# Optimization experiments

Hardware: AMD Instinct MI355X
Metric: run time of the kernel (lower is better)

Reference implementation:

```python
import jax, jax.numpy as jnp
import numpy as np
from jax import lax

NUM_EXPERTS = 64
HIDDEN = 1024
INTERMEDIATE = 768
TOTAL_TOKENS = 8192


def setup_inputs() -> dict:
    key = jax.random.key(0)
    k1, k2, k3, k4 = jax.random.split(key, 4)
    x = jax.random.normal(k1, (TOTAL_TOKENS, HIDDEN), dtype=jnp.float32)
    scale = 0.02
    w1 = jax.random.normal(k2, (NUM_EXPERTS, HIDDEN, INTERMEDIATE), dtype=jnp.float32) * scale
    w2 = jax.random.normal(k3, (NUM_EXPERTS, INTERMEDIATE, HIDDEN), dtype=jnp.float32) * scale
    w3 = jax.random.normal(k4, (NUM_EXPERTS, HIDDEN, INTERMEDIATE), dtype=jnp.float32) * scale
    # Variable tokens per expert, summing exactly to TOTAL_TOKENS (tokens are pre-sorted by expert).
    counts = np.random.default_rng(0).multinomial(TOTAL_TOKENS, [1.0 / NUM_EXPERTS] * NUM_EXPERTS)
    num_tokens_per_expert = jnp.asarray(counts, dtype=jnp.int32)
    return {"x": x, "w1": w1, "w2": w2, "w3": w3,
            "num_tokens_per_expert": num_tokens_per_expert}


def reference(x, w1, w2, w3, num_tokens_per_expert):
    """SwiGLU grouped-expert FFN: down(silu(gate(x)) * up(x)), grouped by expert.

    x: (T, H) tokens sorted by expert; num_tokens_per_expert: (E,) int32.
    Matches torch._grouped_mm semantics: compute in bfloat16, cast back to x.dtype.
    """
    gs = num_tokens_per_expert.astype(jnp.int32)
    xb = x.astype(jnp.bfloat16)
    w1b = w1.astype(jnp.bfloat16)
    w2b = w2.astype(jnp.bfloat16)
    w3b = w3.astype(jnp.bfloat16)
    gate = lax.ragged_dot(xb, w1b, gs)          # (T, I) grouped GEMM
    up = lax.ragged_dot(xb, w3b, gs)            # (T, I)
    h = jax.nn.silu(gate) * up                  # fused SwiGLU activation
    out = lax.ragged_dot(h, w2b, gs)            # (T, H)
    return out.astype(x.dtype)
```

## Files before the change

kernel.cpp:

```cpp
#include <hip/hip_runtime.h>
#include <stdint.h>

#define E_ 64
#define H_ 1024
#define I_ 768
#define T_ 8192

typedef __attribute__((ext_vector_type(4))) float floatx4;
typedef __attribute__((ext_vector_type(8))) short bf16x8;

__device__ inline unsigned short f2bf(float f) {
  union { float f; uint32_t u; } v; v.f = f;
  return (unsigned short)((v.u + 0x7FFFu + ((v.u >> 16) & 1u)) >> 16);
}
__device__ inline float bf2f(unsigned short s) {
  union { uint32_t u; float f; } v; v.u = ((uint32_t)s) << 16;
  return v.f;
}

__device__ inline void gload16(const void* g, void* l) {
  __builtin_amdgcn_global_load_lds(
      (const __attribute__((address_space(1))) void*)g,
      (__attribute__((address_space(3))) void*)l, 16, 0, 0);
}

__global__ void k_prep(const float* __restrict__ x, unsigned short* __restrict__ xb,
                       const int* __restrict__ cnts, int* __restrict__ offs) {
  int i = blockIdx.x * 256 + threadIdx.x;
  float4 v = ((const float4*)x)[i];
  ushort4 o;
  o.x = f2bf(v.x); o.y = f2bf(v.y); o.z = f2bf(v.z); o.w = f2bf(v.w);
  ((ushort4*)xb)[i] = o;
  if (i == 0) {
    int s = 0; offs[0] = 0;
    for (int e = 0; e < E_; ++e) { s += cnts[e]; offs[e + 1] = s; }
  }
}

__global__ __launch_bounds__(256, 2) void k_gemm1(
    const unsigned short* __restrict__ xb, const float* __restrict__ w1,
    const float* __restrict__ w3, unsigned short* __restrict__ h,
    const int* __restrict__ offs) {
  __shared__ unsigned short As[2][256 * 32];
  __shared__ float Bs1[2][32 * 64];
  __shared__ float Bs3[2][32 * 64];

  const int tid = threadIdx.x;
  const int wv = tid >> 6;
  const int l = tid & 63;
  const int lq = l >> 4;
  const int ln = l & 15;
  const int e = blockIdx.x / (I_ / 64);
  const int n0 = (blockIdx.x % (I_ / 64)) * 64;
  const int off = offs[e];
  const int cnt = offs[e + 1] - off;

  const float* b1p = w1 + (size_t)e * (H_ * I_) + (size_t)(tid >> 4) * I_ + n0 + (tid & 15) * 4;
  const float* b3p = w3 + (size_t)e * (H_ * I_) + (size_t)(tid >> 4) * I_ + n0 + (tid & 15) * 4;

  for (int mb = 0; mb < cnt; mb += 256) {
    const int m_here = (cnt - mb) < 256 ? (cnt - mb) : 256;
    const bool active = (wv * 64) < m_here;

    const unsigned short* aptr[4];
#pragma unroll
    for (int r = 0; r < 4; ++r) {
      int row = off + mb + r * 64 + (tid >> 2);
      row = row < (T_ - 1) ? row : (T_ - 1);
      aptr[r] = xb + (size_t)row * H_ + (tid & 3) * 8;
    }

    auto STG = [&](int kt, int buf) {
#pragma unroll
      for (int r = 0; r < 4; ++r)
        gload16(aptr[r] + kt * 32, &As[buf][tid * 8 + r * 2048]);
#pragma unroll
      for (int r = 0; r < 2; ++r) {
        gload16(b1p + (size_t)(kt * 32 + r * 16) * I_, &Bs1[buf][tid * 4 + r * 1024]);
        gload16(b3p + (size_t)(kt * 32 + r * 16) * I_, &Bs3[buf][tid * 4 + r * 1024]);
      }
    };

    floatx4 accG[4][4], accU[4][4];
#pragma unroll
    for (int i2 = 0; i2 < 4; ++i2)
#pragma unroll
      for (int j2 = 0; j2 < 4; ++j2) {
        accG[i2][j2] = (floatx4){0.f, 0.f, 0.f, 0.f};
        accU[i2][j2] = (floatx4){0.f, 0.f, 0.f, 0.f};
      }

    const int NK = H_ / 32;
    STG(0, 0);
    for (int kt = 0; kt < NK; ++kt) {
      const int cur = kt & 1;
      if (kt + 1 < NK) {
        STG(kt + 1, cur ^ 1);
        asm volatile("s_waitcnt vmcnt(8)" ::: "memory");
      } else {
        asm volatile("s_waitcnt vmcnt(0)" ::: "memory");
      }
      __builtin_amdgcn_s_barrier();
      asm volatile("" ::: "memory");

      if (active) {
        const unsigned short* Asc = As[cur];
        const float* B1c = Bs1[cur];
        const float* B3c = Bs3[cur];
        bf16x8 bG[4], bU[4];
#pragma unroll
        for (int nf = 0; nf < 4; ++nf) {
          const float* p1 = &B1c[(lq * 8) * 64 + nf * 16 + ln];
          const float* p3 = &B3c[(lq * 8) * 64 + nf * 16 + ln];
          bf16x8 t1, t3;
#pragma unroll
          for (int j = 0; j < 8; ++j) {
            t1[j] = (short)f2bf(p1[j * 64]);
            t3[j] = (short)f2bf(p3[j * 64]);
          }
          bG[nf] = t1; bU[nf] = t3;
        }
#pragma unroll
        for (int mf = 0; mf < 4; ++mf) {
          const bf16x8 af = *(const bf16x8*)&Asc[(size_t)(wv * 64 + mf * 16 + ln) * 32 + lq * 8];
#pragma unroll
          for (int nf = 0; nf < 4; ++nf) {
            accG[mf][nf] = __builtin_amdgcn_mfma_f32_16x16x32_bf16(af, bG[nf], accG[mf][nf], 0, 0, 0);
            accU[mf][nf] = __builtin_amdgcn_mfma_f32_16x16x32_bf16(af, bU[nf], accU[mf][nf], 0, 0, 0);
          }
        }
      }
      asm volatile("" ::: "memory");
      __builtin_amdgcn_s_barrier();
    }

    if (active) {
#pragma unroll
      for (int mf = 0; mf < 4; ++mf)
#pragma unroll
        for (int nf = 0; nf < 4; ++nf)
#pragma unroll
          for (int r = 0; r < 4; ++r) {
            int row_l = wv * 64 + mf * 16 + lq * 4 + r;
            if (row_l < m_here) {
              float g = bf2f(f2bf(accG[mf][nf][r]));
              float u = bf2f(f2bf(accU[mf][nf][r]));
              float hv = (g / (1.0f + __expf(-g))) * u;
              h[(size_t)(off + mb + row_l) * I_ + n0 + nf * 16 + ln] = f2bf(hv);
            }
          }
    }
    asm volatile("s_waitcnt vmcnt(0)" ::: "memory");
  }
}

__global__ __launch_bounds__(256, 3) void k_gemm2(
    const unsigned short* __restrict__ h, const float* __restrict__ w2,
    float* __restrict__ out, const int* __restrict__ offs) {
  __shared__ unsigned short As[2][256 * 32];
  __shared__ float Bs[2][32 * 64];

  const int tid = threadIdx.x;
  const int wv = tid >> 6;
  const int l = tid & 63;
  const int lq = l >> 4;
  const int ln = l & 15;
  const int e = blockIdx.x / (H_ / 64);
  const int n0 = (blockIdx.x % (H_ / 64)) * 64;
  const int off = offs[e];
  const int cnt = offs[e + 1] - off;

  const float* b2p = w2 + (size_t)e * (I_ * H_) + (size_t)(tid >> 4) * H_ + n0 + (tid & 15) * 4;

  for (int mb = 0; mb < cnt; mb += 256) {
    const int m_here = (cnt - mb) < 256 ? (cnt - mb) : 256;
    const bool active = (wv * 64) < m_here;

    const unsigned short* aptr[4];
#pragma unroll
    for (int r = 0; r < 4; ++r) {
      int row = off + mb + r * 64 + (tid >> 2);
      row = row < (T_ - 1) ? row : (T_ - 1);
      aptr[r] = h + (size_t)row * I_ + (tid & 3) * 8;
    }

    auto STG = [&](int kt, int buf) {
#pragma unroll
      for (int r = 0; r < 4; ++r)
        gload16(aptr[r] + kt * 32, &As[buf][tid * 8 + r * 2048]);
#pragma unroll
      for (int r = 0; r < 2; ++r)
        gload16(b2p + (size_t)(kt * 32 + r * 16) * H_, &Bs[buf][tid * 4 + r * 1024]);
    };

    floatx4 acc[4][4];
#pragma unroll
    for (int i2 = 0; i2 < 4; ++i2)
#pragma unroll
      for (int j2 = 0; j2 < 4; ++j2) acc[i2][j2] = (floatx4){0.f, 0.f, 0.f, 0.f};

    const int NK = I_ / 32;
    STG(0, 0);
    for (int kt = 0; kt < NK; ++kt) {
      const int cur = kt & 1;
      if (kt + 1 < NK) {
        STG(kt + 1, cur ^ 1);
        asm volatile("s_waitcnt vmcnt(6)" ::: "memory");
      } else {
        asm volatile("s_waitcnt vmcnt(0)" ::: "memory");
      }
      __builtin_amdgcn_s_barrier();
      asm volatile("" ::: "memory");

      if (active) {
        const unsigned short* Asc = As[cur];
        const float* Bc = Bs[cur];
        bf16x8 bF[4];
#pragma unroll
        for (int nf = 0; nf < 4; ++nf) {
          const float* p = &Bc[(lq * 8) * 64 + nf * 16 + ln];
          bf16x8 t;
#pragma unroll
          for (int j = 0; j < 8; ++j) t[j] = (short)f2bf(p[j * 64]);
          bF[nf] = t;
        }
#pragma unroll
        for (int mf = 0; mf < 4; ++mf) {
          const bf16x8 af = *(const bf16x8*)&Asc[(size_t)(wv * 64 + mf * 16 + ln) * 32 + lq * 8];
#pragma unroll
          for (int nf = 0; nf < 4; ++nf)
            acc[mf][nf] = __builtin_amdgcn_mfma_f32_16x16x32_bf16(af, bF[nf], acc[mf][nf], 0, 0, 0);
        }
      }
      asm volatile("" ::: "memory");
      __builtin_amdgcn_s_barrier();
    }

    if (active) {
#pragma unroll
      for (int mf = 0; mf < 4; ++mf)
#pragma unroll
        for (int nf = 0; nf < 4; ++nf)
#pragma unroll
          for (int r = 0; r < 4; ++r) {
            int row_l = wv * 64 + mf * 16 + lq * 4 + r;
            if (row_l < m_here)
              out[(size_t)(off + mb + row_l) * H_ + n0 + nf * 16 + ln] = acc[mf][nf][r];
          }
    }
    asm volatile("s_waitcnt vmcnt(0)" ::: "memory");
  }
}

extern "C" void kernel_launch(void* const* d_in, const int* in_sizes, int n_in,
                              void* d_out, int out_size, void* d_ws, size_t ws_size,
                              hipStream_t stream) {
  const float* x  = (const float*)d_in[0];
  const float* w1 = (const float*)d_in[1];
  const float* w2 = (const float*)d_in[2];
  const float* w3 = (const float*)d_in[3];
  const int* cnts = (const int*)d_in[4];
  float* out = (float*)d_out;

  char* ws = (char*)d_ws;
  int* offs = (int*)ws;
  unsigned short* xb = (unsigned short*)(ws + 1024);
  unsigned short* h  = (unsigned short*)(ws + 1024 + (size_t)T_ * H_ * 2);

  k_prep<<<(T_ * H_) / (256 * 4), 256, 0, stream>>>(x, xb, cnts, offs);
  k_gemm1<<<E_ * (I_ / 64), 256, 0, stream>>>(xb, w1, w3, h, offs);
  k_gemm2<<<E_ * (H_ / 64), 256, 0, stream>>>(h, w2, out, offs);
}
```

Before: 628.7 us.

## Load A fragments directly to registers and convert B to bf16 once per tile

Both GEMM kernels stop staging the activation tile in LDS and load A fragments straight from global memory into registers. The fp32 weight tile is converted cooperatively into a swizzled bf16 LDS buffer once per k-step, instead of every wave converting it redundantly. The B prefetch becomes two tiles deep, and the block index is remapped across groups of eight. This cuts LDS footprint and redundant conversion work, but adds a second barrier per k-step and exposes global A-load latency inside the loop.

```diff
diff --git a/kernel.cpp b/kernel.cpp
--- a/kernel.cpp
+++ b/kernel.cpp
@@ -23,6 +23,8 @@
       (const __attribute__((address_space(1))) void*)g,
       (__attribute__((address_space(3))) void*)l, 16, 0, 0);
 }
+
+__device__ inline int bslot(int n, int c) { return n * 4 + (c ^ ((n >> 1) & 3)); }
 
 __global__ void k_prep(const float* __restrict__ x, unsigned short* __restrict__ xb,
                        const int* __restrict__ cnts, int* __restrict__ offs) {
@@ -41,19 +43,22 @@
     const unsigned short* __restrict__ xb, const float* __restrict__ w1,
     const float* __restrict__ w3, unsigned short* __restrict__ h,
     const int* __restrict__ offs) {
-  __shared__ unsigned short As[2][256 * 32];
-  __shared__ float Bs1[2][32 * 64];
-  __shared__ float Bs3[2][32 * 64];
+  __shared__ __align__(16) float Bf[2][2][32 * 64];
+  __shared__ __align__(16) unsigned short Bh[2][64 * 32];
 
   const int tid = threadIdx.x;
   const int wv = tid >> 6;
   const int l = tid & 63;
   const int lq = l >> 4;
   const int ln = l & 15;
-  const int e = blockIdx.x / (I_ / 64);
-  const int n0 = (blockIdx.x % (I_ / 64)) * 64;
+  const int bid = ((int)blockIdx.x & 7) * (E_ * (I_ / 64) / 8) + ((int)blockIdx.x >> 3);
+  const int e = bid / (I_ / 64);
+  const int n0 = (bid % (I_ / 64)) * 64;
   const int off = offs[e];
   const int cnt = offs[e + 1] - off;
+
+  const int cn = tid & 63;
+  const int ck = tid >> 6;
 
   const float* b1p = w1 + (size_t)e * (H_ * I_) + (size_t)(tid >> 4) * I_ + n0 + (tid & 15) * 4;
   const float* b3p = w3 + (size_t)e * (H_ * I_) + (size_t)(tid >> 4) * I_ + n0 + (tid & 15) * 4;
@@ -62,22 +67,19 @@
     const int m_here = (cnt - mb) < 256 ? (cnt - mb) : 256;
     const bool active = (wv * 64) < m_here;
 
-    const unsigned short* aptr[4];
-#pragma unroll
-    for (int r = 0; r < 4; ++r) {
-      int row = off + mb + r * 64 + (tid >> 2);
+    const unsigned short* aF[4];
+#pragma unroll
+    for (int mf = 0; mf < 4; ++mf) {
+      int row = off + mb + wv * 64 + mf * 16 + ln;
       row = row < (T_ - 1) ? row : (T_ - 1);
-      aptr[r] = xb + (size_t)row * H_ + (tid & 3) * 8;
-    }
-
-    auto STG = [&](int kt, int buf) {
-#pragma unroll
-      for (int r = 0; r < 4; ++r)
-        gload16(aptr[r] + kt * 32, &As[buf][tid * 8 + r * 2048]);
+      aF[mf] = xb + (size_t)row * H_ + lq * 8;
+    }
+
+    auto STGB = [&](int kt, int buf) {
 #pragma unroll
       for (int r = 0; r < 2; ++r) {
-        gload16(b1p + (size_t)(kt * 32 + r * 16) * I_, &Bs1[buf][tid * 4 + r * 1024]);
-        gload16(b3p + (size_t)(kt * 32 + r * 16) * I_, &Bs3[buf][tid * 4 + r * 1024]);
+        gload16(b1p + (size_t)(kt * 32 + r * 16) * I_, &Bf[buf][0][tid * 4 + r * 1024]);
+        gload16(b3p + (size_t)(kt * 32 + r * 16) * I_, &Bf[buf][1][tid * 4 + r * 1024]);
       }
     };
 
@@ -91,47 +93,55 @@
       }
 
     const int NK = H_ / 32;
-    STG(0, 0);
+    STGB(0, 0);
+    STGB(1, 1);
     for (int kt = 0; kt < NK; ++kt) {
       const int cur = kt & 1;
-      if (kt + 1 < NK) {
-        STG(kt + 1, cur ^ 1);
-        asm volatile("s_waitcnt vmcnt(8)" ::: "memory");
-      } else {
-        asm volatile("s_waitcnt vmcnt(0)" ::: "memory");
-      }
-      __builtin_amdgcn_s_barrier();
-      asm volatile("" ::: "memory");
-
-      if (active) {
-        const unsigned short* Asc = As[cur];
-        const float* B1c = Bs1[cur];
-        const float* B3c = Bs3[cur];
+      if (kt == NK - 1) asm volatile("s_waitcnt vmcnt(0)" ::: "memory");
+      else              asm volatile("s_waitcnt vmcnt(4)" ::: "memory");
+      __builtin_amdgcn_s_barrier();
+      asm volatile("" ::: "memory");
+
+#pragma unroll
+      for (int m = 0; m < 2; ++m) {
+        uint32_t dw[4];
+#pragma unroll
+        for (int d = 0; d < 4; ++d) {
+          float v0 = Bf[cur][m][(ck * 8 + 2 * d) * 64 + cn];
+          float v1 = Bf[cur][m][(ck * 8 + 2 * d + 1) * 64 + cn];
+          dw[d] = (uint32_t)f2bf(v0) | ((uint32_t)f2bf(v1) << 16);
+        }
+        *(uint4*)&Bh[m][(size_t)bslot(cn, ck) * 8] = make_uint4(dw[0], dw[1], dw[2], dw[3]);
+      }
+      asm volatile("s_waitcnt lgkmcnt(0)" ::: "memory");
+      __builtin_amdgcn_s_barrier();
+      asm volatile("" ::: "memory");
+
+      bf16x8 af[4];
+      if (active) {
+#pragma unroll
+        for (int mf = 0; mf < 4; ++mf) af[mf] = *(const bf16x8*)(aF[mf] + kt * 32);
+      }
+      asm volatile("" ::: "memory");
+      if (kt + 2 < NK) STGB(kt + 2, cur);
+      asm volatile("" ::: "memory");
+
+      if (active) {
         bf16x8 bG[4], bU[4];
 #pragma unroll
         for (int nf = 0; nf < 4; ++nf) {
-          const float* p1 = &B1c[(lq * 8) * 64 + nf * 16 + ln];
-          const float* p3 = &B3c[(lq * 8) * 64 + nf * 16 + ln];
-          bf16x8 t1, t3;
-#pragma unroll
-          for (int j = 0; j < 8; ++j) {
-            t1[j] = (short)f2bf(p1[j * 64]);
-            t3[j] = (short)f2bf(p3[j * 64]);
+          const int sl = bslot(nf * 16 + ln, lq) * 8;
+          bG[nf] = *(const bf16x8*)&Bh[0][sl];
+          bU[nf] = *(const bf16x8*)&Bh[1][sl];
+        }
+#pragma unroll
+        for (int mf = 0; mf < 4; ++mf)
+#pragma unroll
+          for (int nf = 0; nf < 4; ++nf) {
+            accG[mf][nf] = __builtin_amdgcn_mfma_f32_16x16x32_bf16(af[mf], bG[nf], accG[mf][nf], 0, 0, 0);
+            accU[mf][nf] = __builtin_amdgcn_mfma_f32_16x16x32_bf16(af[mf], bU[nf], accU[mf][nf], 0, 0, 0);
           }
-          bG[nf] = t1; bU[nf] = t3;
-        }
-#pragma unroll
-        for (int mf = 0; mf < 4; ++mf) {
-          const bf16x8 af = *(const bf16x8*)&Asc[(size_t)(wv * 64 + mf * 16 + ln) * 32 + lq * 8];
-#pragma unroll
-          for (int nf = 0; nf < 4; ++nf) {
-            accG[mf][nf] = __builtin_amdgcn_mfma_f32_16x16x32_bf16(af, bG[nf], accG[mf][nf], 0, 0, 0);
-            accU[mf][nf] = __builtin_amdgcn_mfma_f32_16x16x32_bf16(af, bU[nf], accU[mf][nf], 0, 0, 0);
-          }
-        }
-      }
-      asm volatile("" ::: "memory");
-      __builtin_amdgcn_s_barrier();
+      }
     }
 
     if (active) {
@@ -157,18 +167,22 @@
 __global__ __launch_bounds__(256, 3) void k_gemm2(
     const unsigned short* __restrict__ h, const float* __restrict__ w2,
     float* __restrict__ out, const int* __restrict__ offs) {
-  __shared__ unsigned short As[2][256 * 32];
-  __shared__ float Bs[2][32 * 64];
+  __shared__ __align__(16) float Bf[2][32 * 64];
+  __shared__ __align__(16) unsigned short Bh[64 * 32];
 
   const int tid = threadIdx.x;
   const int wv = tid >> 6;
   const int l = tid & 63;
   const int lq = l >> 4;
   const int ln = l & 15;
-  const int e = blockIdx.x / (H_ / 64);
-  const int n0 = (blockIdx.x % (H_ / 64)) * 64;
+  const int bid = ((int)blockIdx.x & 7) * (E_ * (H_ / 64) / 8) + ((int)blockIdx.x >> 3);
+  const int e = bid / (H_ / 64);
+  const int n0 = (bid % (H_ / 64)) * 64;
   const int off = offs[e];
   const int cnt = offs[e + 1] - off;
+
+  const int cn = tid & 63;
+  const int ck = tid >> 6;
 
   const float* b2p = w2 + (size_t)e * (I_ * H_) + (size_t)(tid >> 4) * H_ + n0 + (tid & 15) * 4;
 
@@ -176,21 +190,18 @@
     const int m_here = (cnt - mb) < 256 ? (cnt - mb) : 256;
     const bool active = (wv * 64) < m_here;
 
-    const unsigned short* aptr[4];
-#pragma unroll
-    for (int r = 0; r < 4; ++r) {
-      int row = off + mb + r * 64 + (tid >> 2);
+    const unsigned short* aF[4];
+#pragma unroll
+    for (int mf = 0; mf < 4; ++mf) {
+      int row = off + mb + wv * 64 + mf * 16 + ln;
       row = row < (T_ - 1) ? row : (T_ - 1);
-      aptr[r] = h + (size_t)row * I_ + (tid & 3) * 8;
-    }
-
-    auto STG = [&](int kt, int buf) {
-#pragma unroll
-      for (int r = 0; r < 4; ++r)
-        gload16(aptr[r] + kt * 32, &As[buf][tid * 8 + r * 2048]);
+      aF[mf] = h + (size_t)row * I_ + lq * 8;
+    }
+
+    auto STGB = [&](int kt, int buf) {
 #pragma unroll
       for (int r = 0; r < 2; ++r)
-        gload16(b2p + (size_t)(kt * 32 + r * 16) * H_, &Bs[buf][tid * 4 + r * 1024]);
+        gload16(b2p + (size_t)(kt * 32 + r * 16) * H_, &Bf[buf][tid * 4 + r * 1024]);
     };
 
     floatx4 acc[4][4];
@@ -200,40 +211,49 @@
       for (int j2 = 0; j2 < 4; ++j2) acc[i2][j2] = (floatx4){0.f, 0.f, 0.f, 0.f};
 
     const int NK = I_ / 32;
-    STG(0, 0);
+    STGB(0, 0);
+    STGB(1, 1);
     for (int kt = 0; kt < NK; ++kt) {
       const int cur = kt & 1;
-      if (kt + 1 < NK) {
-        STG(kt + 1, cur ^ 1);
-        asm volatile("s_waitcnt vmcnt(6)" ::: "memory");
-      } else {
-        asm volatile("s_waitcnt vmcnt(0)" ::: "memory");
-      }
-      __builtin_amdgcn_s_barrier();
-      asm volatile("" ::: "memory");
-
-      if (active) {
-        const unsigned short* Asc = As[cur];
-        const float* Bc = Bs[cur];
+      if (kt == NK - 1) asm volatile("s_waitcnt vmcnt(0)" ::: "memory");
+      else              asm volatile("s_waitcnt vmcnt(2)" ::: "memory");
+      __builtin_amdgcn_s_barrier();
+      asm volatile("" ::: "memory");
+
+      {
+        uint32_t dw[4];
+#pragma unroll
+        for (int d = 0; d < 4; ++d) {
+          float v0 = Bf[cur][(ck * 8 + 2 * d) * 64 + cn];
+          float v1 = Bf[cur][(ck * 8 + 2 * d + 1) * 64 + cn];
+          dw[d] = (uint32_t)f2bf(v0) | ((uint32_t)f2bf(v1) << 16);
+        }
+        *(uint4*)&Bh[(size_t)bslot(cn, ck) * 8] = make_uint4(dw[0], dw[1], dw[2], dw[3]);
+      }
+      asm volatile("s_waitcnt lgkmcnt(0)" ::: "memory");
+      __builtin_amdgcn_s_barrier();
+      asm volatile("" ::: "memory");
+
+      bf16x8 af[4];
+      if (active) {
+#pragma unroll
+        for (int mf = 0; mf < 4; ++mf) af[mf] = *(const bf16x8*)(aF[mf] + kt * 32);
+      }
+      asm volatile("" ::: "memory");
+      if (kt + 2 < NK) STGB(kt + 2, cur);
+      asm volatile("" ::: "memory");
+
+      if (active) {
         bf16x8 bF[4];
 #pragma unroll
-        for (int nf = 0; nf < 4; ++nf) {
-          const float* p = &Bc[(lq * 8) * 64 + nf * 16 + ln];
-          bf16x8 t;
-#pragma unroll
-          for (int j = 0; j < 8; ++j) t[j] = (short)f2bf(p[j * 64]);
-          bF[nf] = t;
-        }
-#pragma unroll
-        for (int mf = 0; mf < 4; ++mf) {
-          const bf16x8 af = *(const bf16x8*)&Asc[(size_t)(wv * 64 + mf * 16 + ln) * 32 + lq * 8];
+        for (int nf = 0; nf < 4; ++nf)
+          bF[nf] = *(const bf16x8*)&Bh[(size_t)bslot(nf * 16 + ln, lq) * 8];
+#pragma unroll
+        for (int mf = 0; mf < 4; ++mf)
 #pragma unroll
           for (int nf = 0; nf < 4; ++nf)
-            acc[mf][nf] = __builtin_amdgcn_mfma_f32_16x16x32_bf16(af, bF[nf], acc[mf][nf], 0, 0, 0);
-        }
-      }
-      asm volatile("" ::: "memory");
-      __builtin_amdgcn_s_barrier();
+            acc[mf][nf] = __builtin_amdgcn_mfma_f32_16x16x32_bf16(af[mf], bF[nf], acc[mf][nf], 0, 0, 0);
+      }
     }
 
     if (active) {
```

Result: no change. 619.3 us (-1.5%).
